# Kernel optimization log

Measured on AMD Instinct MI355X. Metric: run time of the kernel, lower is better.

The kernel has to match this reference:

```python
import jax, jax.numpy as jnp
import numpy as np

BN_EPS = 1e-5

def _gcn_layer(h, src, dst, W, b, Wr, br, gamma, beta):
    # GraphConv norm='none': sum over in-edges of (X W), plus bias, then ReLU
    m = h @ W                                        # [N, out]
    agg = jax.ops.segment_sum(m[src], dst, num_segments=h.shape[0])
    new = jax.nn.relu(agg + b)
    # residual branch: relu(Linear(h))
    res = jax.nn.relu(h @ Wr + br)
    out = new + res
    # BatchNorm1d over node axis (training-mode batch stats, affine)
    mu = out.mean(axis=0)
    var = out.var(axis=0)
    return (out - mu) * jax.lax.rsqrt(var + BN_EPS) * gamma + beta

def setup_inputs() -> dict:
    key = jax.random.key(0)
    ks = jax.random.split(key, 8)
    N, E, D = 100000, 1600000, 128
    s = 1.0 / np.sqrt(D)
    return {
        "h": jax.random.normal(ks[0], (N, D), jnp.float32),
        "src": jax.random.randint(ks[1], (E,), 0, N, jnp.int32),
        "dst": jax.random.randint(ks[2], (E,), 0, N, jnp.int32),
        "W0": jax.random.normal(ks[3], (D, D), jnp.float32) * s,
        "b0": jnp.zeros((D,), jnp.float32),
        "Wr0": jax.random.normal(ks[4], (D, D), jnp.float32) * s,
        "br0": jnp.zeros((D,), jnp.float32),
        "g0": jnp.ones((D,), jnp.float32),
        "be0": jnp.zeros((D,), jnp.float32),
        "W1": jax.random.normal(ks[5], (D, D), jnp.float32) * s,
        "b1": jnp.zeros((D,), jnp.float32),
        "Wr1": jax.random.normal(ks[6], (D, D), jnp.float32) * s,
        "br1": jnp.zeros((D,), jnp.float32),
        "g1": jnp.ones((D,), jnp.float32),
        "be1": jnp.zeros((D,), jnp.float32),
        "batch_size": 100,
    }

def reference(h, src, dst, W0, b0, Wr0, br0, g0, be0, W1, b1, Wr1, br1, g1, be1, batch_size):
    x = _gcn_layer(h, src, dst, W0, b0, Wr0, br0, g0, be0)
    x = _gcn_layer(x, src, dst, W1, b1, Wr1, br1, g1, be1)
    out_feats = x.shape[-1]
    return x.reshape(batch_size, -1, out_feats)
```

## Files before the change

kernel.cpp:

```cpp
#include <hip/hip_runtime.h>
#include <hip/hip_bf16.h>
#include <hip/hip_fp16.h>

#define D 128

typedef _Float16 h8 __attribute__((ext_vector_type(8)));
typedef float f4 __attribute__((ext_vector_type(4)));


__global__ void hist_kernel(const int* __restrict__ dst, int* __restrict__ counts, int E) {
    for (int e = blockIdx.x * blockDim.x + threadIdx.x; e < E; e += gridDim.x * blockDim.x)
        atomicAdd(&counts[dst[e]], 1);
}

__global__ __launch_bounds__(256) void scan_block_sums(const int* __restrict__ counts,
                                                       int* __restrict__ bsums, int N) {
    __shared__ int sdata[256];
    int t = threadIdx.x;
    int idx = blockIdx.x * 256 + t;
    sdata[t] = (idx < N) ? counts[idx] : 0;
    __syncthreads();
    for (int s = 128; s > 0; s >>= 1) {
        if (t < s) sdata[t] += sdata[t + s];
        __syncthreads();
    }
    if (t == 0) bsums[blockIdx.x] = sdata[0];
}

__global__ __launch_bounds__(1024) void scan_single(int* __restrict__ bsums, int nb,
                                                    int* __restrict__ offsets, int N, int E) {
    __shared__ int sdata[1024];
    int t = threadIdx.x;
    int v = (t < nb) ? bsums[t] : 0;
    sdata[t] = v;
    __syncthreads();
    for (int off = 1; off < 1024; off <<= 1) {
        int u = (t >= off) ? sdata[t - off] : 0;
        __syncthreads();
        sdata[t] += u;
        __syncthreads();
    }
    if (t < nb) bsums[t] = sdata[t] - v;
    if (t == 0) offsets[N] = E;
}

__global__ __launch_bounds__(256) void scan_final(const int* __restrict__ counts,
                                                  const int* __restrict__ bprefix,
                                                  int* __restrict__ offsets, int N) {
    __shared__ int sdata[256];
    int t = threadIdx.x;
    int idx = blockIdx.x * 256 + t;
    int c = (idx < N) ? counts[idx] : 0;
    sdata[t] = c;
    __syncthreads();
    for (int off = 1; off < 256; off <<= 1) {
        int u = (t >= off) ? sdata[t - off] : 0;
        __syncthreads();
        sdata[t] += u;
        __syncthreads();
    }
    if (idx < N) offsets[idx] = bprefix[blockIdx.x] + (sdata[t] - c);
}

__global__ void copy_cursor(const int* __restrict__ offsets, int* __restrict__ cursor, int N) {
    for (int i = blockIdx.x * blockDim.x + threadIdx.x; i < N; i += gridDim.x * blockDim.x)
        cursor[i] = offsets[i];
}

__global__ void fill_csr(const int* __restrict__ src, const int* __restrict__ dst,
                         int* __restrict__ cursor, int* __restrict__ csr, int E) {
    for (int e = blockIdx.x * blockDim.x + threadIdx.x; e < E; e += gridDim.x * blockDim.x) {
        int d = dst[e];
        int p = atomicAdd(&cursor[d], 1);
        csr[p] = src[e];
    }
}


__global__ __launch_bounds__(256) void pack_weights(const float* __restrict__ W,
                                                    const float* __restrict__ Wr,
                                                    const float* __restrict__ br_in,
                                                    const float* __restrict__ bn_sc,
                                                    const float* __restrict__ bn_sh,
                                                    __half* __restrict__ Wp,
                                                    float* __restrict__ cadd,
                                                    float* __restrict__ brp) {
    int t = threadIdx.x;
    for (int slot = t; slot < 4096; slot += 256) {
        int lane = slot & 63;
        int kt = (slot >> 6) & 3;
        int jt = (slot >> 8) & 7;
        int mat = slot >> 11;
        const float* Wsel = mat ? Wr : W;
        int j = jt * 16 + (lane & 15);
        int kb = kt * 32 + (lane >> 4) * 8;
        __half tmp[8];
        #pragma unroll
        for (int e = 0; e < 8; ++e) {
            int k = kb + e;
            float w = Wsel[k * D + j];
            if (bn_sc) w *= bn_sc[k];
            tmp[e] = __float2half(w);
        }
        *(uint4*)&Wp[(size_t)slot * 8] = *(const uint4*)tmp;
    }
    if (t < D) {
        float c = 0.f, bb = br_in[t];
        if (bn_sh) {
            for (int k = 0; k < D; ++k) {
                float sh = bn_sh[k];
                c += sh * W[k * D + t];
                bb += sh * Wr[k * D + t];
            }
        }
        cadd[t] = c;
        brp[t] = bb;
    }
}


template <bool XHALF>
__global__ __launch_bounds__(256) void gemm_mfma(const void* __restrict__ x,
                                                 const __half* __restrict__ Wp,
                                                 const float* __restrict__ cadd,
                                                 const float* __restrict__ brp,
                                                 __half* __restrict__ m,
                                                 __half* __restrict__ r, int N) {
    int wv = threadIdx.x >> 6, lane = threadIdx.x & 63;
    int tilebase = blockIdx.x * 64 + wv * 16;
    int kgrp = lane >> 4;
    int arow = tilebase + (lane & 15);
    bool rowok = arow < N;

    h8 a0v = 0, a1v = 0, a2v = 0, a3v = 0;
    if (rowok) {
        if constexpr (XHALF) {
            const __half* xp = (const __half*)x + (size_t)arow * D + kgrp * 8;
            a0v = *(const h8*)(xp + 0);
            a1v = *(const h8*)(xp + 32);
            a2v = *(const h8*)(xp + 64);
            a3v = *(const h8*)(xp + 96);
        } else {
            const float* xf = (const float*)x + (size_t)arow * D + kgrp * 8;
            #pragma unroll
            for (int kt = 0; kt < 4; ++kt) {
                f4 lo = *(const f4*)(xf + kt * 32);
                f4 hi = *(const f4*)(xf + kt * 32 + 4);
                h8 tv;
                tv[0] = (_Float16)lo[0]; tv[1] = (_Float16)lo[1];
                tv[2] = (_Float16)lo[2]; tv[3] = (_Float16)lo[3];
                tv[4] = (_Float16)hi[0]; tv[5] = (_Float16)hi[1];
                tv[6] = (_Float16)hi[2]; tv[7] = (_Float16)hi[3];
                if (kt == 0) a0v = tv; else if (kt == 1) a1v = tv;
                else if (kt == 2) a2v = tv; else a3v = tv;
            }
        }
    }

    f4 accm[8], accr[8];
    #pragma unroll
    for (int jt = 0; jt < 8; ++jt) { accm[jt] = 0; accr[jt] = 0; }

    const h8* wp = (const h8*)Wp;
    #pragma unroll
    for (int jt = 0; jt < 8; ++jt) {
        const h8* bm = wp + ((size_t)jt * 4) * 64 + lane;
        const h8* bw = wp + ((size_t)(8 + jt) * 4) * 64 + lane;
        accm[jt] = __builtin_amdgcn_mfma_f32_16x16x32_f16(a0v, bm[0 * 64], accm[jt], 0, 0, 0);
        accm[jt] = __builtin_amdgcn_mfma_f32_16x16x32_f16(a1v, bm[1 * 64], accm[jt], 0, 0, 0);
        accm[jt] = __builtin_amdgcn_mfma_f32_16x16x32_f16(a2v, bm[2 * 64], accm[jt], 0, 0, 0);
        accm[jt] = __builtin_amdgcn_mfma_f32_16x16x32_f16(a3v, bm[3 * 64], accm[jt], 0, 0, 0);
        accr[jt] = __builtin_amdgcn_mfma_f32_16x16x32_f16(a0v, bw[0 * 64], accr[jt], 0, 0, 0);
        accr[jt] = __builtin_amdgcn_mfma_f32_16x16x32_f16(a1v, bw[1 * 64], accr[jt], 0, 0, 0);
        accr[jt] = __builtin_amdgcn_mfma_f32_16x16x32_f16(a2v, bw[2 * 64], accr[jt], 0, 0, 0);
        accr[jt] = __builtin_amdgcn_mfma_f32_16x16x32_f16(a3v, bw[3 * 64], accr[jt], 0, 0, 0);
    }

    int j0 = lane & 15;
    int orow0 = tilebase + kgrp * 4;
    #pragma unroll
    for (int jt = 0; jt < 8; ++jt) {
        int j = jt * 16 + j0;
        float cm = cadd[j];
        float bb = brp[j];
        #pragma unroll
        for (int q = 0; q < 4; ++q) {
            int row = orow0 + q;
            if (row < N) {
                m[(size_t)row * D + j] = __float2half(accm[jt][q] + cm);
                r[(size_t)row * D + j] = __float2half(fmaxf(accr[jt][q] + bb, 0.f));
            }
        }
    }
}


template <bool OHALF>
__global__ __launch_bounds__(256) void combine_kernel(const __half* __restrict__ m,
                                                      const int* __restrict__ csr,
                                                      const int* __restrict__ offsets,
                                                      const float* __restrict__ bias,
                                                      const __half* __restrict__ r,
                                                      void* __restrict__ out,
                                                      float* __restrict__ stats, int N) {
    __shared__ float4 sred[4][64];
    int t = threadIdx.x;
    int wave = t >> 6, lane = t & 63;
    int node = blockIdx.x * 4 + wave;
    float v0 = 0.f, v1 = 0.f;
    if (node < N) {
        int e0 = offsets[node], e1 = offsets[node + 1];
        const uint* mp = (const uint*)m;
        float a0 = 0.f, a1 = 0.f, b0 = 0.f, b1 = 0.f;
        float c0 = 0.f, c1 = 0.f, d0 = 0.f, d1 = 0.f;
        int e = e0;
        for (; e + 4 <= e1; e += 4) {
            int s0 = csr[e], s1 = csr[e + 1], s2 = csr[e + 2], s3 = csr[e + 3];
            uint p0 = mp[(size_t)s0 * 64 + lane];
            uint p1 = mp[(size_t)s1 * 64 + lane];
            uint p2 = mp[(size_t)s2 * 64 + lane];
            uint p3 = mp[(size_t)s3 * 64 + lane];
            float2 f0 = __half22float2(*reinterpret_cast<__half2*>(&p0));
            float2 f1 = __half22float2(*reinterpret_cast<__half2*>(&p1));
            float2 f2 = __half22float2(*reinterpret_cast<__half2*>(&p2));
            float2 f3 = __half22float2(*reinterpret_cast<__half2*>(&p3));
            a0 += f0.x; a1 += f0.y;
            b0 += f1.x; b1 += f1.y;
            c0 += f2.x; c1 += f2.y;
            d0 += f3.x; d1 += f3.y;
        }
        for (; e < e1; ++e) {
            int s = csr[e];
            uint p = mp[(size_t)s * 64 + lane];
            float2 f = __half22float2(*reinterpret_cast<__half2*>(&p));
            a0 += f.x; a1 += f.y;
        }
        float sum0 = (a0 + b0) + (c0 + d0);
        float sum1 = (a1 + b1) + (c1 + d1);
        uint rv = ((const uint*)r)[(size_t)node * 64 + lane];
        float2 rf = __half22float2(*reinterpret_cast<__half2*>(&rv));
        float2 bv = *(const float2*)&bias[2 * lane];
        v0 = fmaxf(sum0 + bv.x, 0.f) + rf.x;
        v1 = fmaxf(sum1 + bv.y, 0.f) + rf.y;
        if constexpr (OHALF) {
            __half2 hv = __floats2half2_rn(v0, v1);
            ((uint*)out)[(size_t)node * 64 + lane] = *reinterpret_cast<uint*>(&hv);
        } else {
            *(float2*)&((float*)out)[(size_t)node * D + 2 * lane] = make_float2(v0, v1);
        }
    }
    sred[wave][lane] = make_float4(v0, v1, v0 * v0, v1 * v1);
    __syncthreads();
    if (wave == 0) {
        float4 q0 = sred[0][lane], q1 = sred[1][lane], q2 = sred[2][lane], q3 = sred[3][lane];
        int copy = blockIdx.x & 7;
        float* ss = &stats[copy * 128];
        float* sq = &stats[1024 + copy * 128];
        atomicAdd(&ss[2 * lane],     q0.x + q1.x + q2.x + q3.x);
        atomicAdd(&ss[2 * lane + 1], q0.y + q1.y + q2.y + q3.y);
        atomicAdd(&sq[2 * lane],     q0.z + q1.z + q2.z + q3.z);
        atomicAdd(&sq[2 * lane + 1], q0.w + q1.w + q2.w + q3.w);
    }
}


__global__ void bn_finalize(float* __restrict__ stats, const float* __restrict__ g,
                            const float* __restrict__ be, float invN) {
    int j = threadIdx.x;
    float s = 0.f, q = 0.f;
    #pragma unroll
    for (int c = 0; c < 8; ++c) {
        s += stats[c * 128 + j];
        q += stats[1024 + c * 128 + j];
    }
    float mu = s * invN;
    float var = q * invN - mu * mu;
    float sc = g[j] * rsqrtf(var + 1e-5f);
    stats[2048 + j] = sc;
    stats[2048 + 128 + j] = be[j] - mu * sc;
}

__global__ __launch_bounds__(256) void bn_apply(float* __restrict__ buf,
                                                const float* __restrict__ stats, int n4) {
    for (int i = blockIdx.x * blockDim.x + threadIdx.x; i < n4; i += gridDim.x * blockDim.x) {
        float4 v = ((const float4*)buf)[i];
        int c0 = (i * 4) & 127;
        float4 sc = *(const float4*)&stats[2048 + c0];
        float4 sh = *(const float4*)&stats[2048 + 128 + c0];
        v.x = v.x * sc.x + sh.x;
        v.y = v.y * sc.y + sh.y;
        v.z = v.z * sc.z + sh.z;
        v.w = v.w * sc.w + sh.w;
        ((float4*)buf)[i] = v;
    }
}


static inline char* align_up(char* p, size_t a) {
    return (char*)(((uintptr_t)p + (a - 1)) & ~(uintptr_t)(a - 1));
}

extern "C" void kernel_launch(void* const* d_in, const int* in_sizes, int n_in,
                              void* d_out, int out_size, void* d_ws, size_t ws_size,
                              hipStream_t stream) {
    const float* h   = (const float*)d_in[0];
    const int*   src = (const int*)d_in[1];
    const int*   dst = (const int*)d_in[2];
    const float* W0  = (const float*)d_in[3];
    const float* b0  = (const float*)d_in[4];
    const float* Wr0 = (const float*)d_in[5];
    const float* br0 = (const float*)d_in[6];
    const float* g0  = (const float*)d_in[7];
    const float* be0 = (const float*)d_in[8];
    const float* W1  = (const float*)d_in[9];
    const float* b1  = (const float*)d_in[10];
    const float* Wr1 = (const float*)d_in[11];
    const float* br1 = (const float*)d_in[12];
    const float* g1  = (const float*)d_in[13];
    const float* be1 = (const float*)d_in[14];

    const int N = in_sizes[0] / D;
    const int E = in_sizes[1];
    float* out = (float*)d_out;

    char* p = (char*)d_ws;
    __half* m_buf  = (__half*)p;              p += (size_t)N * D * sizeof(__half);
    p = align_up(p, 256);
    __half* x1_buf = (__half*)p;              p += (size_t)N * D * sizeof(__half);
    p = align_up(p, 256);
    __half* r_buf  = (__half*)p;              p += (size_t)N * D * sizeof(__half);
    p = align_up(p, 256);
    int* counts  = (int*)p;                   p += (size_t)N * sizeof(int);
    p = align_up(p, 256);
    int* offsets = (int*)p;                   p += (size_t)(N + 1) * sizeof(int);
    p = align_up(p, 256);
    int* cursor  = (int*)p;                   p += (size_t)N * sizeof(int);
    p = align_up(p, 256);
    int* bsums   = (int*)p;                   p += 1024 * sizeof(int);
    p = align_up(p, 256);
    int* csr     = (int*)p;                   p += (size_t)E * sizeof(int);
    p = align_up(p, 256);
    float* stats1 = (float*)p;                p += 2304 * sizeof(float);
    p = align_up(p, 256);
    float* stats2 = (float*)p;                p += 2304 * sizeof(float);
    p = align_up(p, 256);
    __half* Wp0 = (__half*)p;                 p += 32768 * sizeof(__half);
    p = align_up(p, 256);
    __half* Wp1 = (__half*)p;                 p += 32768 * sizeof(__half);
    p = align_up(p, 256);
    float* cadd0 = (float*)p;                 p += D * sizeof(float);
    float* brp0  = (float*)p;                 p += D * sizeof(float);
    float* cadd1 = (float*)p;                 p += D * sizeof(float);
    float* brp1  = (float*)p;                 p += D * sizeof(float);
    (void)ws_size;

    const int nb = (N + 255) / 256;
    const float invN = 1.0f / (float)N;

    hipMemsetAsync(counts, 0, (size_t)N * sizeof(int), stream);
    hist_kernel<<<2048, 256, 0, stream>>>(dst, counts, E);
    scan_block_sums<<<nb, 256, 0, stream>>>(counts, bsums, N);
    scan_single<<<1, 1024, 0, stream>>>(bsums, nb, offsets, N, E);
    scan_final<<<nb, 256, 0, stream>>>(counts, bsums, offsets, N);
    copy_cursor<<<512, 256, 0, stream>>>(offsets, cursor, N);
    fill_csr<<<2048, 256, 0, stream>>>(src, dst, cursor, csr, E);

    const int gemm_grid = (N + 63) / 64;
    const int comb_grid = (N + 3) / 4;
    const int n4 = N * D / 4;

    pack_weights<<<1, 256, 0, stream>>>(W0, Wr0, br0, nullptr, nullptr, Wp0, cadd0, brp0);
    gemm_mfma<false><<<gemm_grid, 256, 0, stream>>>(h, Wp0, cadd0, brp0, m_buf, r_buf, N);
    hipMemsetAsync(stats1, 0, 2048 * sizeof(float), stream);
    combine_kernel<true><<<comb_grid, 256, 0, stream>>>(m_buf, csr, offsets, b0, r_buf,
                                                        x1_buf, stats1, N);
    bn_finalize<<<1, D, 0, stream>>>(stats1, g0, be0, invN);

    pack_weights<<<1, 256, 0, stream>>>(W1, Wr1, br1, stats1 + 2048, stats1 + 2048 + 128,
                                        Wp1, cadd1, brp1);
    gemm_mfma<true><<<gemm_grid, 256, 0, stream>>>(x1_buf, Wp1, cadd1, brp1, m_buf, r_buf, N);
    hipMemsetAsync(stats2, 0, 2048 * sizeof(float), stream);
    combine_kernel<false><<<comb_grid, 256, 0, stream>>>(m_buf, csr, offsets, b1, r_buf,
                                                         out, stats2, N);
    bn_finalize<<<1, D, 0, stream>>>(stats2, g1, be1, invN);
    bn_apply<<<2048, 256, 0, stream>>>(out, stats2, n4);
}
```

Baseline: 789.6 us.

## Split neighbor aggregation into two column-half passes with shuffled CSR indices

The neighbor-gather combine kernel becomes two launches, each covering 64 of the 128 feature columns. Each wave loads 64 CSR indices cooperatively and broadcasts them with shuffles, so the two half-waves gather alternating edges, and their partial sums are merged with a cross-half shuffle. The intent is to halve the gathered working set per pass for better cache reuse and more memory parallelism. The cost is reading the CSR and offsets twice and issuing extra launches. Separately, the cursor copy is folded into the final scan kernel, removing one launch.

```diff
diff --git a/kernel.cpp b/kernel.cpp
--- a/kernel.cpp
+++ b/kernel.cpp
@@ -46,7 +46,8 @@
 
 __global__ __launch_bounds__(256) void scan_final(const int* __restrict__ counts,
                                                   const int* __restrict__ bprefix,
-                                                  int* __restrict__ offsets, int N) {
+                                                  int* __restrict__ offsets,
+                                                  int* __restrict__ cursor, int N) {
     __shared__ int sdata[256];
     int t = threadIdx.x;
     int idx = blockIdx.x * 256 + t;
@@ -59,12 +60,11 @@
         sdata[t] += u;
         __syncthreads();
     }
-    if (idx < N) offsets[idx] = bprefix[blockIdx.x] + (sdata[t] - c);
-}
-
-__global__ void copy_cursor(const int* __restrict__ offsets, int* __restrict__ cursor, int N) {
-    for (int i = blockIdx.x * blockDim.x + threadIdx.x; i < N; i += gridDim.x * blockDim.x)
-        cursor[i] = offsets[i];
+    if (idx < N) {
+        int v = bprefix[blockIdx.x] + (sdata[t] - c);
+        offsets[idx] = v;
+        cursor[idx] = v;
+    }
 }
 
 __global__ void fill_csr(const int* __restrict__ src, const int* __restrict__ dst,
@@ -196,70 +196,94 @@
 
 
 template <bool OHALF>
-__global__ __launch_bounds__(256) void combine_kernel(const __half* __restrict__ m,
-                                                      const int* __restrict__ csr,
-                                                      const int* __restrict__ offsets,
-                                                      const float* __restrict__ bias,
-                                                      const __half* __restrict__ r,
-                                                      void* __restrict__ out,
-                                                      float* __restrict__ stats, int N) {
-    __shared__ float4 sred[4][64];
+__global__ __launch_bounds__(256) void combine_split(const __half* __restrict__ m,
+                                                     const int* __restrict__ csr,
+                                                     const int* __restrict__ offsets,
+                                                     const float* __restrict__ bias,
+                                                     const __half* __restrict__ r,
+                                                     void* __restrict__ out,
+                                                     float* __restrict__ stats,
+                                                     int N, int pass) {
+    __shared__ float4 sred[4][32];
     int t = threadIdx.x;
     int wave = t >> 6, lane = t & 63;
+    int hf = lane >> 5, l = lane & 31;
     int node = blockIdx.x * 4 + wave;
+    int coloff = pass * 32 + l;
+
     float v0 = 0.f, v1 = 0.f;
     if (node < N) {
         int e0 = offsets[node], e1 = offsets[node + 1];
         const uint* mp = (const uint*)m;
         float a0 = 0.f, a1 = 0.f, b0 = 0.f, b1 = 0.f;
         float c0 = 0.f, c1 = 0.f, d0 = 0.f, d1 = 0.f;
-        int e = e0;
-        for (; e + 4 <= e1; e += 4) {
-            int s0 = csr[e], s1 = csr[e + 1], s2 = csr[e + 2], s3 = csr[e + 3];
-            uint p0 = mp[(size_t)s0 * 64 + lane];
-            uint p1 = mp[(size_t)s1 * 64 + lane];
-            uint p2 = mp[(size_t)s2 * 64 + lane];
-            uint p3 = mp[(size_t)s3 * 64 + lane];
-            float2 f0 = __half22float2(*reinterpret_cast<__half2*>(&p0));
-            float2 f1 = __half22float2(*reinterpret_cast<__half2*>(&p1));
-            float2 f2 = __half22float2(*reinterpret_cast<__half2*>(&p2));
-            float2 f3 = __half22float2(*reinterpret_cast<__half2*>(&p3));
-            a0 += f0.x; a1 += f0.y;
-            b0 += f1.x; b1 += f1.y;
-            c0 += f2.x; c1 += f2.y;
-            d0 += f3.x; d1 += f3.y;
-        }
-        for (; e < e1; ++e) {
-            int s = csr[e];
-            uint p = mp[(size_t)s * 64 + lane];
-            float2 f = __half22float2(*reinterpret_cast<__half2*>(&p));
-            a0 += f.x; a1 += f.y;
+        for (int base = e0; base < e1; base += 64) {
+            int idx = 0;
+            if (base + lane < e1) idx = csr[base + lane];
+            int nav = min(64, e1 - base);
+            int i = 0;
+            int nfull = (nav >> 3) << 2;
+            for (; i < nfull; i += 4) {
+                int s0 = __shfl(idx, 2 * i + hf);
+                int s1 = __shfl(idx, 2 * i + 2 + hf);
+                int s2 = __shfl(idx, 2 * i + 4 + hf);
+                int s3 = __shfl(idx, 2 * i + 6 + hf);
+                uint p0 = mp[(size_t)s0 * 64 + coloff];
+                uint p1 = mp[(size_t)s1 * 64 + coloff];
+                uint p2 = mp[(size_t)s2 * 64 + coloff];
+                uint p3 = mp[(size_t)s3 * 64 + coloff];
+                float2 f0 = __half22float2(*reinterpret_cast<__half2*>(&p0));
+                float2 f1 = __half22float2(*reinterpret_cast<__half2*>(&p1));
+                float2 f2 = __half22float2(*reinterpret_cast<__half2*>(&p2));
+                float2 f3 = __half22float2(*reinterpret_cast<__half2*>(&p3));
+                a0 += f0.x; a1 += f0.y;
+                b0 += f1.x; b1 += f1.y;
+                c0 += f2.x; c1 += f2.y;
+                d0 += f3.x; d1 += f3.y;
+            }
+            for (; 2 * i < nav; ++i) {
+                int j = 2 * i + hf;
+                int s = __shfl(idx, j);
+                if (j < nav) {
+                    uint p = mp[(size_t)s * 64 + coloff];
+                    float2 f = __half22float2(*reinterpret_cast<__half2*>(&p));
+                    a0 += f.x; a1 += f.y;
+                }
+            }
         }
         float sum0 = (a0 + b0) + (c0 + d0);
         float sum1 = (a1 + b1) + (c1 + d1);
-        uint rv = ((const uint*)r)[(size_t)node * 64 + lane];
+        sum0 += __shfl_xor(sum0, 32);
+        sum1 += __shfl_xor(sum1, 32);
+        uint rv = ((const uint*)r)[(size_t)node * 64 + coloff];
         float2 rf = __half22float2(*reinterpret_cast<__half2*>(&rv));
-        float2 bv = *(const float2*)&bias[2 * lane];
+        float2 bv = *(const float2*)&bias[2 * coloff];
         v0 = fmaxf(sum0 + bv.x, 0.f) + rf.x;
         v1 = fmaxf(sum1 + bv.y, 0.f) + rf.y;
-        if constexpr (OHALF) {
-            __half2 hv = __floats2half2_rn(v0, v1);
-            ((uint*)out)[(size_t)node * 64 + lane] = *reinterpret_cast<uint*>(&hv);
-        } else {
-            *(float2*)&((float*)out)[(size_t)node * D + 2 * lane] = make_float2(v0, v1);
-        }
-    }
-    sred[wave][lane] = make_float4(v0, v1, v0 * v0, v1 * v1);
+        if (hf == 0) {
+            if constexpr (OHALF) {
+                __half2 hv = __floats2half2_rn(v0, v1);
+                ((uint*)out)[(size_t)node * 64 + coloff] = *reinterpret_cast<uint*>(&hv);
+            } else {
+                *(float2*)&((float*)out)[(size_t)node * D + 2 * coloff] = make_float2(v0, v1);
+            }
+        }
+    }
+    if (hf == 0) sred[wave][l] = make_float4(v0, v1, v0 * v0, v1 * v1);
     __syncthreads();
     if (wave == 0) {
-        float4 q0 = sred[0][lane], q1 = sred[1][lane], q2 = sred[2][lane], q3 = sred[3][lane];
+        float4 q0 = sred[0][l], q1 = sred[1][l], q2 = sred[2][l], q3 = sred[3][l];
         int copy = blockIdx.x & 7;
-        float* ss = &stats[copy * 128];
-        float* sq = &stats[1024 + copy * 128];
-        atomicAdd(&ss[2 * lane],     q0.x + q1.x + q2.x + q3.x);
-        atomicAdd(&ss[2 * lane + 1], q0.y + q1.y + q2.y + q3.y);
-        atomicAdd(&sq[2 * lane],     q0.z + q1.z + q2.z + q3.z);
-        atomicAdd(&sq[2 * lane + 1], q0.w + q1.w + q2.w + q3.w);
+        int col = pass * 64 + 2 * l;
+        if (hf == 0) {
+            float* ss = &stats[copy * 128 + col];
+            atomicAdd(&ss[0], q0.x + q1.x + q2.x + q3.x);
+            atomicAdd(&ss[1], q0.y + q1.y + q2.y + q3.y);
+        } else {
+            float* sq = &stats[1024 + copy * 128 + col];
+            atomicAdd(&sq[0], q0.z + q1.z + q2.z + q3.z);
+            atomicAdd(&sq[1], q0.w + q1.w + q2.w + q3.w);
+        }
     }
 }
 
@@ -361,8 +385,7 @@
     hist_kernel<<<2048, 256, 0, stream>>>(dst, counts, E);
     scan_block_sums<<<nb, 256, 0, stream>>>(counts, bsums, N);
     scan_single<<<1, 1024, 0, stream>>>(bsums, nb, offsets, N, E);
-    scan_final<<<nb, 256, 0, stream>>>(counts, bsums, offsets, N);
-    copy_cursor<<<512, 256, 0, stream>>>(offsets, cursor, N);
+    scan_final<<<nb, 256, 0, stream>>>(counts, bsums, offsets, cursor, N);
     fill_csr<<<2048, 256, 0, stream>>>(src, dst, cursor, csr, E);
 
     const int gemm_grid = (N + 63) / 64;
@@ -372,16 +395,20 @@
     pack_weights<<<1, 256, 0, stream>>>(W0, Wr0, br0, nullptr, nullptr, Wp0, cadd0, brp0);
     gemm_mfma<false><<<gemm_grid, 256, 0, stream>>>(h, Wp0, cadd0, brp0, m_buf, r_buf, N);
     hipMemsetAsync(stats1, 0, 2048 * sizeof(float), stream);
-    combine_kernel<true><<<comb_grid, 256, 0, stream>>>(m_buf, csr, offsets, b0, r_buf,
-                                                        x1_buf, stats1, N);
+    combine_split<true><<<comb_grid, 256, 0, stream>>>(m_buf, csr, offsets, b0, r_buf,
+                                                       x1_buf, stats1, N, 0);
+    combine_split<true><<<comb_grid, 256, 0, stream>>>(m_buf, csr, offsets, b0, r_buf,
+                                                       x1_buf, stats1, N, 1);
     bn_finalize<<<1, D, 0, stream>>>(stats1, g0, be0, invN);
 
     pack_weights<<<1, 256, 0, stream>>>(W1, Wr1, br1, stats1 + 2048, stats1 + 2048 + 128,
                                         Wp1, cadd1, brp1);
     gemm_mfma<true><<<gemm_grid, 256, 0, stream>>>(x1_buf, Wp1, cadd1, brp1, m_buf, r_buf, N);
     hipMemsetAsync(stats2, 0, 2048 * sizeof(float), stream);
-    combine_kernel<false><<<comb_grid, 256, 0, stream>>>(m_buf, csr, offsets, b1, r_buf,
-                                                         out, stats2, N);
+    combine_split<false><<<comb_grid, 256, 0, stream>>>(m_buf, csr, offsets, b1, r_buf,
+                                                        out, stats2, N, 0);
+    combine_split<false><<<comb_grid, 256, 0, stream>>>(m_buf, csr, offsets, b1, r_buf,
+                                                        out, stats2, N, 1);
     bn_finalize<<<1, D, 0, stream>>>(stats2, g1, be1, invN);
     bn_apply<<<2048, 256, 0, stream>>>(out, stats2, n4);
 }
```

Measured after the change: 1.088 ms. 37.8% more time.

## Aggregate features before GEMM and fuse GEMM with bias, residual and BN stats

Applied to the files above, without the earlier changes.

Reorders the layer as (A·X)·W instead of A·(X·W). Neighbour features are gathered into an fp16 agg buffer first, then one MFMA kernel computes both agg·W and x·Wr, applies bias, ReLU, the residual add and the BN-shift correction scaled by in-degree, and accumulates the BN statistics. This removes the separate m and r intermediate buffers and the combine pass. It adds a standalone fp32-to-fp16 conversion of the input and merges cursor initialisation into the scan kernel. Summing fp16 inputs before the GEMM changes rounding, and the gather loop is unrolled by 2 instead of 4.

```diff
diff --git a/kernel.cpp b/kernel.cpp
--- a/kernel.cpp
+++ b/kernel.cpp
@@ -46,7 +46,8 @@
 
 __global__ __launch_bounds__(256) void scan_final(const int* __restrict__ counts,
                                                   const int* __restrict__ bprefix,
-                                                  int* __restrict__ offsets, int N) {
+                                                  int* __restrict__ offsets,
+                                                  int* __restrict__ cursor, int N) {
     __shared__ int sdata[256];
     int t = threadIdx.x;
     int idx = blockIdx.x * 256 + t;
@@ -59,12 +60,11 @@
         sdata[t] += u;
         __syncthreads();
     }
-    if (idx < N) offsets[idx] = bprefix[blockIdx.x] + (sdata[t] - c);
-}
-
-__global__ void copy_cursor(const int* __restrict__ offsets, int* __restrict__ cursor, int N) {
-    for (int i = blockIdx.x * blockDim.x + threadIdx.x; i < N; i += gridDim.x * blockDim.x)
-        cursor[i] = offsets[i];
+    if (idx < N) {
+        int v = bprefix[blockIdx.x] + (sdata[t] - c);
+        offsets[idx] = v;
+        cursor[idx] = v;
+    }
 }
 
 __global__ void fill_csr(const int* __restrict__ src, const int* __restrict__ dst,
@@ -73,6 +73,20 @@
         int d = dst[e];
         int p = atomicAdd(&cursor[d], 1);
         csr[p] = src[e];
+    }
+}
+
+
+__global__ __launch_bounds__(256) void convert_f16(const float* __restrict__ in,
+                                                   __half* __restrict__ out, int n4) {
+    for (int i = blockIdx.x * blockDim.x + threadIdx.x; i < n4; i += gridDim.x * blockDim.x) {
+        float4 v = ((const float4*)in)[i];
+        __half2 h0 = __floats2half2_rn(v.x, v.y);
+        __half2 h1 = __floats2half2_rn(v.z, v.w);
+        uint2 u;
+        u.x = *reinterpret_cast<uint*>(&h0);
+        u.y = *reinterpret_cast<uint*>(&h1);
+        ((uint2*)out)[i] = u;
     }
 }
 
@@ -119,42 +133,69 @@
 }
 
 
-template <bool XHALF>
-__global__ __launch_bounds__(256) void gemm_mfma(const void* __restrict__ x,
-                                                 const __half* __restrict__ Wp,
-                                                 const float* __restrict__ cadd,
-                                                 const float* __restrict__ brp,
-                                                 __half* __restrict__ m,
-                                                 __half* __restrict__ r, int N) {
+__global__ __launch_bounds__(256) void gather_sum(const __half* __restrict__ x,
+                                                  const int* __restrict__ csr,
+                                                  const int* __restrict__ offsets,
+                                                  __half* __restrict__ agg, int N) {
+    int t = threadIdx.x;
+    int wave = t >> 6, lane = t & 63;
+    int node = blockIdx.x * 4 + wave;
+    if (node >= N) return;
+    int e0 = offsets[node], e1 = offsets[node + 1];
+    const uint* mp = (const uint*)x;
+    float a0 = 0.f, a1 = 0.f, c0 = 0.f, c1 = 0.f;
+    int e = e0;
+    for (; e + 2 <= e1; e += 2) {
+        int s0 = csr[e], s1 = csr[e + 1];
+        uint p0 = mp[(size_t)s0 * 64 + lane];
+        uint p1 = mp[(size_t)s1 * 64 + lane];
+        float2 f0 = __half22float2(*reinterpret_cast<__half2*>(&p0));
+        float2 f1 = __half22float2(*reinterpret_cast<__half2*>(&p1));
+        a0 += f0.x; a1 += f0.y;
+        c0 += f1.x; c1 += f1.y;
+    }
+    if (e < e1) {
+        int s = csr[e];
+        uint p = mp[(size_t)s * 64 + lane];
+        float2 f = __half22float2(*reinterpret_cast<__half2*>(&p));
+        a0 += f.x; a1 += f.y;
+    }
+    __half2 hv = __floats2half2_rn(a0 + c0, a1 + c1);
+    ((uint*)agg)[(size_t)node * 64 + lane] = *reinterpret_cast<uint*>(&hv);
+}
+
+
+template <bool OHALF>
+__global__ __launch_bounds__(256) void gemm_fused(const __half* __restrict__ x,
+                                                  const __half* __restrict__ agg,
+                                                  const __half* __restrict__ Wp,
+                                                  const float* __restrict__ cadd,
+                                                  const float* __restrict__ brp,
+                                                  const float* __restrict__ bvec,
+                                                  const int* __restrict__ counts,
+                                                  void* __restrict__ outbuf,
+                                                  float* __restrict__ stats, int N) {
+    __shared__ float sds[4][8][16];
+    __shared__ float sdq[4][8][16];
     int wv = threadIdx.x >> 6, lane = threadIdx.x & 63;
     int tilebase = blockIdx.x * 64 + wv * 16;
-    int kgrp = lane >> 4;
-    int arow = tilebase + (lane & 15);
+    int kgrp = lane >> 4, j0 = lane & 15;
+    int arow = tilebase + j0;
     bool rowok = arow < N;
 
-    h8 a0v = 0, a1v = 0, a2v = 0, a3v = 0;
+    h8 ax0 = 0, ax1 = 0, ax2 = 0, ax3 = 0;
+    h8 ag0 = 0, ag1 = 0, ag2 = 0, ag3 = 0;
     if (rowok) {
-        if constexpr (XHALF) {
-            const __half* xp = (const __half*)x + (size_t)arow * D + kgrp * 8;
-            a0v = *(const h8*)(xp + 0);
-            a1v = *(const h8*)(xp + 32);
-            a2v = *(const h8*)(xp + 64);
-            a3v = *(const h8*)(xp + 96);
-        } else {
-            const float* xf = (const float*)x + (size_t)arow * D + kgrp * 8;
-            #pragma unroll
-            for (int kt = 0; kt < 4; ++kt) {
-                f4 lo = *(const f4*)(xf + kt * 32);
-                f4 hi = *(const f4*)(xf + kt * 32 + 4);
-                h8 tv;
-                tv[0] = (_Float16)lo[0]; tv[1] = (_Float16)lo[1];
-                tv[2] = (_Float16)lo[2]; tv[3] = (_Float16)lo[3];
-                tv[4] = (_Float16)hi[0]; tv[5] = (_Float16)hi[1];
-                tv[6] = (_Float16)hi[2]; tv[7] = (_Float16)hi[3];
-                if (kt == 0) a0v = tv; else if (kt == 1) a1v = tv;
-                else if (kt == 2) a2v = tv; else a3v = tv;
-            }
-        }
+        const __half* xp = x + (size_t)arow * D + kgrp * 8;
+        ax0 = *(const h8*)(xp + 0);
+        ax1 = *(const h8*)(xp + 32);
+        ax2 = *(const h8*)(xp + 64);
+        ax3 = *(const h8*)(xp + 96);
+        const __half* ap = agg + (size_t)arow * D + kgrp * 8;
+        ag0 = *(const h8*)(ap + 0);
+        ag1 = *(const h8*)(ap + 32);
+        ag2 = *(const h8*)(ap + 64);
+        ag3 = *(const h8*)(ap + 96);
     }
 
     f4 accm[8], accr[8];
@@ -166,100 +207,76 @@
     for (int jt = 0; jt < 8; ++jt) {
         const h8* bm = wp + ((size_t)jt * 4) * 64 + lane;
         const h8* bw = wp + ((size_t)(8 + jt) * 4) * 64 + lane;
-        accm[jt] = __builtin_amdgcn_mfma_f32_16x16x32_f16(a0v, bm[0 * 64], accm[jt], 0, 0, 0);
-        accm[jt] = __builtin_amdgcn_mfma_f32_16x16x32_f16(a1v, bm[1 * 64], accm[jt], 0, 0, 0);
-        accm[jt] = __builtin_amdgcn_mfma_f32_16x16x32_f16(a2v, bm[2 * 64], accm[jt], 0, 0, 0);
-        accm[jt] = __builtin_amdgcn_mfma_f32_16x16x32_f16(a3v, bm[3 * 64], accm[jt], 0, 0, 0);
-        accr[jt] = __builtin_amdgcn_mfma_f32_16x16x32_f16(a0v, bw[0 * 64], accr[jt], 0, 0, 0);
-        accr[jt] = __builtin_amdgcn_mfma_f32_16x16x32_f16(a1v, bw[1 * 64], accr[jt], 0, 0, 0);
-        accr[jt] = __builtin_amdgcn_mfma_f32_16x16x32_f16(a2v, bw[2 * 64], accr[jt], 0, 0, 0);
-        accr[jt] = __builtin_amdgcn_mfma_f32_16x16x32_f16(a3v, bw[3 * 64], accr[jt], 0, 0, 0);
-    }
-
-    int j0 = lane & 15;
+        accm[jt] = __builtin_amdgcn_mfma_f32_16x16x32_f16(ag0, bm[0 * 64], accm[jt], 0, 0, 0);
+        accm[jt] = __builtin_amdgcn_mfma_f32_16x16x32_f16(ag1, bm[1 * 64], accm[jt], 0, 0, 0);
+        accm[jt] = __builtin_amdgcn_mfma_f32_16x16x32_f16(ag2, bm[2 * 64], accm[jt], 0, 0, 0);
+        accm[jt] = __builtin_amdgcn_mfma_f32_16x16x32_f16(ag3, bm[3 * 64], accm[jt], 0, 0, 0);
+        accr[jt] = __builtin_amdgcn_mfma_f32_16x16x32_f16(ax0, bw[0 * 64], accr[jt], 0, 0, 0);
+        accr[jt] = __builtin_amdgcn_mfma_f32_16x16x32_f16(ax1, bw[1 * 64], accr[jt], 0, 0, 0);
+        accr[jt] = __builtin_amdgcn_mfma_f32_16x16x32_f16(ax2, bw[2 * 64], accr[jt], 0, 0, 0);
+        accr[jt] = __builtin_amdgcn_mfma_f32_16x16x32_f16(ax3, bw[3 * 64], accr[jt], 0, 0, 0);
+    }
+
     int orow0 = tilebase + kgrp * 4;
+    float dg[4];
+    #pragma unroll
+    for (int q = 0; q < 4; ++q) {
+        int row = orow0 + q;
+        dg[q] = (row < N) ? (float)counts[row] : 0.f;
+    }
+
+    float ls[8], lq[8];
     #pragma unroll
     for (int jt = 0; jt < 8; ++jt) {
         int j = jt * 16 + j0;
         float cm = cadd[j];
         float bb = brp[j];
+        float bj = bvec[j];
+        float s = 0.f, qq = 0.f;
         #pragma unroll
         for (int q = 0; q < 4; ++q) {
             int row = orow0 + q;
+            float o = 0.f;
             if (row < N) {
-                m[(size_t)row * D + j] = __float2half(accm[jt][q] + cm);
-                r[(size_t)row * D + j] = __float2half(fmaxf(accr[jt][q] + bb, 0.f));
+                float nw = fmaxf(accm[jt][q] + dg[q] * cm + bj, 0.f);
+                float rs = fmaxf(accr[jt][q] + bb, 0.f);
+                o = nw + rs;
+                if constexpr (OHALF) {
+                    ((__half*)outbuf)[(size_t)row * D + j] = __float2half(o);
+                } else {
+                    ((float*)outbuf)[(size_t)row * D + j] = o;
+                }
             }
+            s += o;
+            qq += o * o;
         }
-    }
-}
-
-
-template <bool OHALF>
-__global__ __launch_bounds__(256) void combine_kernel(const __half* __restrict__ m,
-                                                      const int* __restrict__ csr,
-                                                      const int* __restrict__ offsets,
-                                                      const float* __restrict__ bias,
-                                                      const __half* __restrict__ r,
-                                                      void* __restrict__ out,
-                                                      float* __restrict__ stats, int N) {
-    __shared__ float4 sred[4][64];
-    int t = threadIdx.x;
-    int wave = t >> 6, lane = t & 63;
-    int node = blockIdx.x * 4 + wave;
-    float v0 = 0.f, v1 = 0.f;
-    if (node < N) {
-        int e0 = offsets[node], e1 = offsets[node + 1];
-        const uint* mp = (const uint*)m;
-        float a0 = 0.f, a1 = 0.f, b0 = 0.f, b1 = 0.f;
-        float c0 = 0.f, c1 = 0.f, d0 = 0.f, d1 = 0.f;
-        int e = e0;
-        for (; e + 4 <= e1; e += 4) {
-            int s0 = csr[e], s1 = csr[e + 1], s2 = csr[e + 2], s3 = csr[e + 3];
-            uint p0 = mp[(size_t)s0 * 64 + lane];
-            uint p1 = mp[(size_t)s1 * 64 + lane];
-            uint p2 = mp[(size_t)s2 * 64 + lane];
-            uint p3 = mp[(size_t)s3 * 64 + lane];
-            float2 f0 = __half22float2(*reinterpret_cast<__half2*>(&p0));
-            float2 f1 = __half22float2(*reinterpret_cast<__half2*>(&p1));
-            float2 f2 = __half22float2(*reinterpret_cast<__half2*>(&p2));
-            float2 f3 = __half22float2(*reinterpret_cast<__half2*>(&p3));
-            a0 += f0.x; a1 += f0.y;
-            b0 += f1.x; b1 += f1.y;
-            c0 += f2.x; c1 += f2.y;
-            d0 += f3.x; d1 += f3.y;
+        ls[jt] = s;
+        lq[jt] = qq;
+    }
+
+    #pragma unroll
+    for (int jt = 0; jt < 8; ++jt) {
+        ls[jt] += __shfl_xor(ls[jt], 16);
+        ls[jt] += __shfl_xor(ls[jt], 32);
+        lq[jt] += __shfl_xor(lq[jt], 16);
+        lq[jt] += __shfl_xor(lq[jt], 32);
+    }
+    if (lane < 16) {
+        #pragma unroll
+        for (int jt = 0; jt < 8; ++jt) {
+            sds[wv][jt][j0] = ls[jt];
+            sdq[wv][jt][j0] = lq[jt];
         }
-        for (; e < e1; ++e) {
-            int s = csr[e];
-            uint p = mp[(size_t)s * 64 + lane];
-            float2 f = __half22float2(*reinterpret_cast<__half2*>(&p));
-            a0 += f.x; a1 += f.y;
-        }
-        float sum0 = (a0 + b0) + (c0 + d0);
-        float sum1 = (a1 + b1) + (c1 + d1);
-        uint rv = ((const uint*)r)[(size_t)node * 64 + lane];
-        float2 rf = __half22float2(*reinterpret_cast<__half2*>(&rv));
-        float2 bv = *(const float2*)&bias[2 * lane];
-        v0 = fmaxf(sum0 + bv.x, 0.f) + rf.x;
-        v1 = fmaxf(sum1 + bv.y, 0.f) + rf.y;
-        if constexpr (OHALF) {
-            __half2 hv = __floats2half2_rn(v0, v1);
-            ((uint*)out)[(size_t)node * 64 + lane] = *reinterpret_cast<uint*>(&hv);
-        } else {
-            *(float2*)&((float*)out)[(size_t)node * D + 2 * lane] = make_float2(v0, v1);
-        }
-    }
-    sred[wave][lane] = make_float4(v0, v1, v0 * v0, v1 * v1);
+    }
     __syncthreads();
-    if (wave == 0) {
-        float4 q0 = sred[0][lane], q1 = sred[1][lane], q2 = sred[2][lane], q3 = sred[3][lane];
+    int tt = threadIdx.x;
+    if (tt < 128) {
+        int jj0 = tt & 15, jjt = tt >> 4;
+        float s = sds[0][jjt][jj0] + sds[1][jjt][jj0] + sds[2][jjt][jj0] + sds[3][jjt][jj0];
+        float q = sdq[0][jjt][jj0] + sdq[1][jjt][jj0] + sdq[2][jjt][jj0] + sdq[3][jjt][jj0];
         int copy = blockIdx.x & 7;
-        float* ss = &stats[copy * 128];
-        float* sq = &stats[1024 + copy * 128];
-        atomicAdd(&ss[2 * lane],     q0.x + q1.x + q2.x + q3.x);
-        atomicAdd(&ss[2 * lane + 1], q0.y + q1.y + q2.y + q3.y);
-        atomicAdd(&sq[2 * lane],     q0.z + q1.z + q2.z + q3.z);
-        atomicAdd(&sq[2 * lane + 1], q0.w + q1.w + q2.w + q3.w);
+        atomicAdd(&stats[copy * 128 + tt], s);
+        atomicAdd(&stats[1024 + copy * 128 + tt], q);
     }
 }
 
@@ -324,11 +341,11 @@
     float* out = (float*)d_out;
 
     char* p = (char*)d_ws;
-    __half* m_buf  = (__half*)p;              p += (size_t)N * D * sizeof(__half);
+    __half* x0_buf = (__half*)p;              p += (size_t)N * D * sizeof(__half);
     p = align_up(p, 256);
     __half* x1_buf = (__half*)p;              p += (size_t)N * D * sizeof(__half);
     p = align_up(p, 256);
-    __half* r_buf  = (__half*)p;              p += (size_t)N * D * sizeof(__half);
+    __half* agg_buf = (__half*)p;             p += (size_t)N * D * sizeof(__half);
     p = align_up(p, 256);
     int* counts  = (int*)p;                   p += (size_t)N * sizeof(int);
     p = align_up(p, 256);
@@ -357,12 +374,13 @@
     const int nb = (N + 255) / 256;
     const float invN = 1.0f / (float)N;
 
+    convert_f16<<<2048, 256, 0, stream>>>(h, x0_buf, N * D / 4);
+
     hipMemsetAsync(counts, 0, (size_t)N * sizeof(int), stream);
     hist_kernel<<<2048, 256, 0, stream>>>(dst, counts, E);
     scan_block_sums<<<nb, 256, 0, stream>>>(counts, bsums, N);
     scan_single<<<1, 1024, 0, stream>>>(bsums, nb, offsets, N, E);
-    scan_final<<<nb, 256, 0, stream>>>(counts, bsums, offsets, N);
-    copy_cursor<<<512, 256, 0, stream>>>(offsets, cursor, N);
+    scan_final<<<nb, 256, 0, stream>>>(counts, bsums, offsets, cursor, N);
     fill_csr<<<2048, 256, 0, stream>>>(src, dst, cursor, csr, E);
 
     const int gemm_grid = (N + 63) / 64;
@@ -370,18 +388,18 @@
     const int n4 = N * D / 4;
 
     pack_weights<<<1, 256, 0, stream>>>(W0, Wr0, br0, nullptr, nullptr, Wp0, cadd0, brp0);
-    gemm_mfma<false><<<gemm_grid, 256, 0, stream>>>(h, Wp0, cadd0, brp0, m_buf, r_buf, N);
+    gather_sum<<<comb_grid, 256, 0, stream>>>(x0_buf, csr, offsets, agg_buf, N);
     hipMemsetAsync(stats1, 0, 2048 * sizeof(float), stream);
-    combine_kernel<true><<<comb_grid, 256, 0, stream>>>(m_buf, csr, offsets, b0, r_buf,
-                                                        x1_buf, stats1, N);
+    gemm_fused<true><<<gemm_grid, 256, 0, stream>>>(x0_buf, agg_buf, Wp0, cadd0, brp0,
+                                                    b0, counts, x1_buf, stats1, N);
     bn_finalize<<<1, D, 0, stream>>>(stats1, g0, be0, invN);
 
     pack_weights<<<1, 256, 0, stream>>>(W1, Wr1, br1, stats1 + 2048, stats1 + 2048 + 128,
                                         Wp1, cadd1, brp1);
-    gemm_mfma<true><<<gemm_grid, 256, 0, stream>>>(x1_buf, Wp1, cadd1, brp1, m_buf, r_buf, N);
+    gather_sum<<<comb_grid, 256, 0, stream>>>(x1_buf, csr, offsets, agg_buf, N);
     hipMemsetAsync(stats2, 0, 2048 * sizeof(float), stream);
-    combine_kernel<false><<<comb_grid, 256, 0, stream>>>(m_buf, csr, offsets, b1, r_buf,
-                                                         out, stats2, N);
+    gemm_fused<false><<<gemm_grid, 256, 0, stream>>>(x1_buf, agg_buf, Wp1, cadd1, brp1,
+                                                     b1, counts, out, stats2, N);
     bn_finalize<<<1, D, 0, stream>>>(stats2, g1, be1, invN);
     bn_apply<<<2048, 256, 0, stream>>>(out, stats2, n4);
 }
```

New measurement: 703.9 us. 1.12x faster.
